# Kernel tuning notes

Measured on AMD Instinct MI355X. Metric: run time of the kernel, lower is better.

The kernel has to match this reference:

```python
import jax, jax.numpy as jnp
from jax import lax
import numpy as np

B, C, FH, FW, H, V, L = 256, 512, 8, 16, 512, 64, 24


def setup_inputs() -> dict:
    key = jax.random.key(0)
    ks = jax.random.split(key, 32)
    s = 0.05
    n = lambda k, shp: jax.random.normal(k, shp, dtype=jnp.float32) * s
    return {
        "encoder_ftrs": jax.random.normal(ks[0], (B, C, FH, FW), dtype=jnp.float32),
        "sequences": jax.random.randint(ks[1], (B, L), 0, V),
        "test": 0,
        "embed_w": n(ks[2], (V, H)),
        "init_state": n(ks[3], (2, 1, H)),
        "attn_W_w": n(ks[4], (H, C)), "attn_W_b": jnp.zeros((H,), jnp.float32),
        "attn_U_w": n(ks[5], (H, H)), "attn_U_b": jnp.zeros((H,), jnp.float32),
        "attn_v_w": n(ks[6], (1, H)), "attn_v_b": jnp.zeros((1,), jnp.float32),
        "fc_w": n(ks[7], (H, C + H)), "fc_b": jnp.zeros((H,), jnp.float32),
        "cls_w": n(ks[8], (V, H)), "cls_b": jnp.zeros((V,), jnp.float32),
        "gru0_wih": n(ks[9], (3 * H, 2 * H)), "gru0_whh": n(ks[10], (3 * H, H)),
        "gru0_bih": jnp.zeros((3 * H,), jnp.float32), "gru0_bhh": jnp.zeros((3 * H,), jnp.float32),
        "gru1_wih": n(ks[11], (3 * H, H)), "gru1_whh": n(ks[12], (3 * H, H)),
        "gru1_bih": jnp.zeros((3 * H,), jnp.float32), "gru1_bhh": jnp.zeros((3 * H,), jnp.float32),
    }


def _gru_cell(x, h, wih, whh, bih, bhh):
    # PyTorch GRUCell: r,z gates then candidate n with r applied on hidden path
    gi = x @ wih.T + bih
    gh = h @ whh.T + bhh
    i_r, i_z, i_n = jnp.split(gi, 3, axis=-1)
    h_r, h_z, h_n = jnp.split(gh, 3, axis=-1)
    r = jax.nn.sigmoid(i_r + h_r)
    z = jax.nn.sigmoid(i_z + h_z)
    nact = jnp.tanh(i_n + r * h_n)
    return (1.0 - z) * nact + z * h


def reference(encoder_ftrs, sequences, test, embed_w, init_state,
              attn_W_w, attn_W_b, attn_U_w, attn_U_b, attn_v_w, attn_v_b,
              fc_w, fc_b, cls_w, cls_b,
              gru0_wih, gru0_whh, gru0_bih, gru0_bhh,
              gru1_wih, gru1_whh, gru1_bih, gru1_bhh):
    bsz = encoder_ftrs.shape[0]
    # [B, L_sp, C] encoder states
    states = encoder_ftrs.reshape(bsz, C, -1).transpose(0, 2, 1)
    # attn_W(states) is timestep-independent: precompute once (same math)
    Ws = states @ attn_W_w.T + attn_W_b  # [B, L_sp, H]

    def apply_attn(h_top):
        e = jax.nn.relu(Ws + (h_top @ attn_U_w.T + attn_U_b)[:, None, :])
        scores = e @ attn_v_w[0] + attn_v_b[0]          # [B, L_sp]
        a = jax.nn.softmax(scores, axis=-1)
        ctx = jnp.einsum('bl,blc->bc', a, states)        # [B, C]
        return ctx

    def out_proj(ctx, h_top):
        return jax.nn.relu(jnp.concatenate([ctx, h_top], axis=-1) @ fc_w.T + fc_b)

    xs = embed_w[sequences[:, :-1]]                      # [B, T, H]
    h0 = jnp.broadcast_to(init_state, (2, bsz, H))       # repeat over batch
    y0 = out_proj(apply_attn(h0[1]), h0[1])              # time_step == -1 (output dropped)

    def step(carry, x_t):
        h, y = carry
        h_l0 = _gru_cell(jnp.concatenate([y, x_t], axis=-1), h[0],
                         gru0_wih, gru0_whh, gru0_bih, gru0_bhh)
        h_l1 = _gru_cell(h_l0, h[1], gru1_wih, gru1_whh, gru1_bih, gru1_bhh)
        hn = jnp.stack([h_l0, h_l1], axis=0)
        yn = out_proj(apply_attn(h_l1), h_l1)
        return (hn, yn), yn

    _, ys = lax.scan(step, (h0, y0), xs.transpose(1, 0, 2))   # [T, B, H]
    logits = ys.transpose(1, 0, 2) @ cls_w.T + cls_b          # [B, T, V]

    labels = sequences[:, 1:]
    mask = (labels > 0).astype(logits.dtype)
    logp = jax.nn.log_softmax(logits, axis=-1)
    nll = -jnp.take_along_axis(logp, labels[..., None], axis=-1)[..., 0]
    loss = jnp.sum(nll * mask) / jnp.sum(mask)
    return loss
```

## Files before the change

### kernel.cpp

```cpp
#include <hip/hip_runtime.h>
#include <hip/hip_bf16.h>
#include <cstddef>

#define BB 256
#define CC 512
#define SS 128
#define HH 512
#define VV 64
#define LL 24

typedef unsigned short ush;
typedef __attribute__((ext_vector_type(8))) short short8;
typedef __attribute__((ext_vector_type(4))) float f32x4;

__device__ __forceinline__ float wave_sum(float v) {
#pragma unroll
    for (int off = 32; off > 0; off >>= 1) v += __shfl_xor(v, off);
    return v;
}
__device__ __forceinline__ float wave_max(float v) {
#pragma unroll
    for (int off = 32; off > 0; off >>= 1) v = fmaxf(v, __shfl_xor(v, off));
    return v;
}
__device__ __forceinline__ float sigm(float x) { return 1.0f / (1.0f + expf(-x)); }
__device__ __forceinline__ ush f2bf(float f) {
    unsigned u = __float_as_uint(f);
    u += 0x7FFFu + ((u >> 16) & 1u);
    return (ush)(u >> 16);
}
__device__ __forceinline__ float bf2f(ush b) {
    return __uint_as_float(((unsigned)b) << 16);
}
__device__ __forceinline__ unsigned pack2(float a, float b) {
    return (unsigned)f2bf(a) | ((unsigned)f2bf(b) << 16);
}

__global__ __launch_bounds__(256) void init_kernel(const float* __restrict__ init_state,
                                                   float* __restrict__ h0,
                                                   float* __restrict__ h1,
                                                   ush* __restrict__ h0b,
                                                   ush* __restrict__ h1b,
                                                   float* __restrict__ acc) {
    int idx = blockIdx.x * 256 + threadIdx.x;
    if (idx < BB * HH) {
        float a = init_state[idx & (HH - 1)];
        float b = init_state[HH + (idx & (HH - 1))];
        h0[idx] = a; h1[idx] = b;
        h0b[idx] = f2bf(a); h1b[idx] = f2bf(b);
    }
    if (idx < 2) acc[idx] = 0.0f;
}

__global__ __launch_bounds__(256) void conv_kernel(const float* __restrict__ src,
                                                   ush* __restrict__ dst, int n4) {
    int i = blockIdx.x * 256 + threadIdx.x;
    if (i < n4) {
        float4 v = ((const float4*)src)[i];
        uint2 o;
        o.x = pack2(v.x, v.y);
        o.y = pack2(v.z, v.w);
        ((uint2*)dst)[i] = o;
    }
}

__global__ __launch_bounds__(128) void gather_kernel(const float* __restrict__ embed_w,
                                                     const int* __restrict__ seq,
                                                     ush* __restrict__ xall) {
    int item = blockIdx.x;
    int t = item >> 8, m = item & 255;
    int row = seq[m * LL + t];
    float4 v = ((const float4*)(embed_w + (size_t)row * HH))[threadIdx.x];
    uint2 o;
    o.x = pack2(v.x, v.y);
    o.y = pack2(v.z, v.w);
    ((uint2*)(xall + (size_t)item * HH))[threadIdx.x] = o;
}

__global__ __launch_bounds__(256) void enc_conv(const float* __restrict__ enc,
                                                ush* __restrict__ enc_t) {
    int b = blockIdx.x, cg = blockIdx.y;
    int c0 = cg * 128;
    __shared__ ush tile[128][130];
    const float* src = enc + ((size_t)b * 512 + c0) * 128;
#pragma unroll
    for (int i = 0; i < 16; i++) {
        int lin = i * 256 + threadIdx.x;
        int cl = lin >> 5, s4 = lin & 31;
        float4 v = ((const float4*)(src + (size_t)cl * 128))[s4];
        ush b0 = f2bf(v.x), b1 = f2bf(v.y), b2 = f2bf(v.z), b3 = f2bf(v.w);
        tile[s4 * 4 + 0][cl] = b0;
        tile[s4 * 4 + 1][cl] = b1;
        tile[s4 * 4 + 2][cl] = b2;
        tile[s4 * 4 + 3][cl] = b3;
    }
    __syncthreads();
#pragma unroll
    for (int i = 0; i < 16; i++) {
        int lin = i * 256 + threadIdx.x;
        int sl = lin >> 5, c4 = lin & 31;
        ush a0 = tile[sl][c4 * 4 + 0], a1 = tile[sl][c4 * 4 + 1];
        ush a2 = tile[sl][c4 * 4 + 2], a3 = tile[sl][c4 * 4 + 3];
        uint2 o;
        o.x = (unsigned)a0 | ((unsigned)a1 << 16);
        o.y = (unsigned)a2 | ((unsigned)a3 << 16);
        ((uint2*)(enc_t + ((size_t)b * 128 + sl) * 512 + c0))[c4] = o;
    }
}

__global__ __launch_bounds__(256) void ws_v2(const ush* __restrict__ enc_t,
                                             const ush* __restrict__ Wb,
                                             const float* __restrict__ bias,
                                             ush* __restrict__ Ws_bf) {
    int tid = threadIdx.x;
    int wave = tid >> 6, lane = tid & 63;
    int quad = lane >> 4, l16 = lane & 15;
    int m0 = blockIdx.x * 128 + wave * 32;
    int n0 = blockIdx.y * 128;
    const ush* ap = enc_t + (size_t)(m0 + l16) * 512 + quad * 8;
    const ush* bp = Wb + (size_t)(n0 + l16) * 512 + quad * 8;
    f32x4 acc[2][8];
#pragma unroll
    for (int f = 0; f < 2; f++)
#pragma unroll
        for (int s = 0; s < 8; s++) acc[f][s] = (f32x4){0.f, 0.f, 0.f, 0.f};
    short8 ac[2], bc[8], an[2], bn[8];
    ac[0] = *(const short8*)(ap);
    ac[1] = *(const short8*)(ap + (size_t)16 * 512);
#pragma unroll
    for (int s = 0; s < 8; s++) bc[s] = *(const short8*)(bp + (size_t)s * 16 * 512);
#pragma unroll
    for (int ks = 0; ks < 16; ks++) {
        if (ks < 15) {
            int k = (ks + 1) * 32;
            an[0] = *(const short8*)(ap + k);
            an[1] = *(const short8*)(ap + (size_t)16 * 512 + k);
#pragma unroll
            for (int s = 0; s < 8; s++)
                bn[s] = *(const short8*)(bp + (size_t)s * 16 * 512 + k);
        }
#pragma unroll
        for (int f = 0; f < 2; f++)
#pragma unroll
            for (int s = 0; s < 8; s++)
                acc[f][s] = __builtin_amdgcn_mfma_f32_16x16x32_bf16(ac[f], bc[s], acc[f][s], 0, 0, 0);
        if (ks < 15) {
            ac[0] = an[0]; ac[1] = an[1];
#pragma unroll
            for (int s = 0; s < 8; s++) bc[s] = bn[s];
        }
    }
#pragma unroll
    for (int s = 0; s < 8; s++) {
        int n = n0 + s * 16 + l16;
        float bs = bias[n];
#pragma unroll
        for (int f = 0; f < 2; f++)
#pragma unroll
            for (int r = 0; r < 4; r++) {
                int m = m0 + f * 16 + quad * 4 + r;
                Ws_bf[(size_t)m * HH + n] = f2bf(acc[f][s][r] + bs);
            }
    }
}

template <int NSTEP>
__device__ __forceinline__ void segk(const ush* __restrict__ ap,
                                     const ush* __restrict__ bp,
                                     size_t wofs, f32x4& a0, f32x4& a1) {
    short8 as[4], bs0[4], bs1[4];
    constexpr int PRE = NSTEP < 4 ? NSTEP : 4;
#pragma unroll
    for (int i = 0; i < PRE; i++) {
        as[i]  = *(const short8*)(ap + 32 * i);
        bs0[i] = *(const short8*)(bp + 32 * i);
        bs1[i] = *(const short8*)(bp + wofs + 32 * i);
    }
#pragma unroll
    for (int i = 0; i < NSTEP; i++) {
        const int sl = i & 3;
        a0 = __builtin_amdgcn_mfma_f32_16x16x32_bf16(as[sl], bs0[sl], a0, 0, 0, 0);
        a1 = __builtin_amdgcn_mfma_f32_16x16x32_bf16(as[sl], bs1[sl], a1, 0, 0, 0);
        if (i + 4 < NSTEP) {
            as[sl]  = *(const short8*)(ap + 32 * (i + 4));
            bs0[sl] = *(const short8*)(bp + 32 * (i + 4));
            bs1[sl] = *(const short8*)(bp + wofs + 32 * (i + 4));
        }
    }
}

struct GruArgs {
    const ush* xs[8][2];
    const ush* wb[8][2];
    int wst[8][2];
    int nks[8][2];
    int slot[8][2];
    int zmask;
};

__global__ __launch_bounds__(512) void gru_fused(GruArgs A,
                                                 const float* __restrict__ h_prev,
                                                 const float* __restrict__ bih,
                                                 const float* __restrict__ bhh,
                                                 float* __restrict__ h_out,
                                                 ush* __restrict__ h_out_bf) {
    int tid = threadIdx.x;
    int wave = __builtin_amdgcn_readfirstlane(tid >> 6);
    int lane = tid & 63, quad = lane >> 4, l16 = lane & 15;
    int m0 = blockIdx.x * 16, n0 = blockIdx.y * 32;
    __shared__ float gbuf[10][16][32];
    if (A.zmask) {
        int mi = tid >> 5, ni = tid & 31;
#pragma unroll
        for (int s = 0; s < 10; s++)
            if ((A.zmask >> s) & 1) gbuf[s][mi][ni] = 0.0f;
    }
    for (int e = 0; e < 2; e++) {
        int nks = A.nks[wave][e];
        if (nks == 0) continue;
        f32x4 a0 = (f32x4){0.f, 0.f, 0.f, 0.f};
        f32x4 a1 = (f32x4){0.f, 0.f, 0.f, 0.f};
        int wst = A.wst[wave][e];
        const ush* ap = A.xs[wave][e] + (size_t)(m0 + l16) * 512 + quad * 8;
        const ush* bp = A.wb[wave][e] + (size_t)(n0 + l16) * wst + quad * 8;
        size_t wofs = (size_t)16 * wst;
        if (nks == 16) segk<16>(ap, bp, wofs, a0, a1);
        else           segk<8>(ap, bp, wofs, a0, a1);
        int sl = A.slot[wave][e];
#pragma unroll
        for (int r = 0; r < 4; r++) {
            gbuf[sl][quad * 4 + r][l16]      = a0[r];
            gbuf[sl][quad * 4 + r][16 + l16] = a1[r];
        }
    }
    __syncthreads();
    {
        int mi = tid >> 5, ni = tid & 31;
        int n = n0 + ni;
        size_t off = (size_t)(m0 + mi) * HH + n;
        float r  = sigm(gbuf[0][mi][ni] + gbuf[1][mi][ni] + gbuf[2][mi][ni] +
                        bih[n] + bhh[n]);
        float zf = sigm(gbuf[3][mi][ni] + gbuf[4][mi][ni] + gbuf[5][mi][ni] +
                        bih[512 + n] + bhh[512 + n]);
        float na = tanhf(gbuf[6][mi][ni] + gbuf[7][mi][ni] + bih[1024 + n] +
                         r * (gbuf[8][mi][ni] + gbuf[9][mi][ni] + bhh[1024 + n]));
        float hp = h_prev[off];
        float ho = (1.0f - zf) * na + zf * hp;
        h_out[off] = ho;
        h_out_bf[off] = f2bf(ho);
    }
}

__global__ __launch_bounds__(512) void fc_fused(const ush* __restrict__ ctx,
                                                const ush* __restrict__ h,
                                                const ush* __restrict__ wFc,
                                                const float* __restrict__ bias,
                                                ush* __restrict__ y,
                                                ush* __restrict__ ys) {
    int tid = threadIdx.x;
    int wave = __builtin_amdgcn_readfirstlane(tid >> 6);
    int lane = tid & 63, quad = lane >> 4, l16 = lane & 15;
    int m0 = blockIdx.x * 16, n0 = blockIdx.y * 32;
    const ush* X = (wave < 4) ? ctx : h;
    int q = wave & 3;
    f32x4 a0 = (f32x4){0.f, 0.f, 0.f, 0.f};
    f32x4 a1 = (f32x4){0.f, 0.f, 0.f, 0.f};
    const ush* ap = X + (size_t)(m0 + l16) * 512 + q * 128 + quad * 8;
    const ush* bp = wFc + (size_t)(n0 + l16) * 1024 + (wave >= 4 ? 512 : 0) + q * 128 + quad * 8;
    segk<4>(ap, bp, (size_t)16 * 1024, a0, a1);
    __shared__ float gbuf[8][16][32];
#pragma unroll
    for (int r = 0; r < 4; r++) {
        gbuf[wave][quad * 4 + r][l16]      = a0[r];
        gbuf[wave][quad * 4 + r][16 + l16] = a1[r];
    }
    __syncthreads();
    {
        int mi = tid >> 5, ni = tid & 31;
        int n = n0 + ni;
        float v = bias[n];
#pragma unroll
        for (int w = 0; w < 8; w++) v += gbuf[w][mi][ni];
        v = fmaxf(v, 0.0f);
        ush bb = f2bf(v);
        size_t off = (size_t)(m0 + mi) * HH + n;
        y[off] = bb;
        if (ys) ys[off] = bb;
    }
}

__global__ __launch_bounds__(512) void u_fused(const ush* __restrict__ h,
                                               const ush* __restrict__ wU,
                                               const float* __restrict__ Ub,
                                               float* __restrict__ Uo) {
    int tid = threadIdx.x;
    int wave = __builtin_amdgcn_readfirstlane(tid >> 6);
    int lane = tid & 63, quad = lane >> 4, l16 = lane & 15;
    int m0 = blockIdx.x * 16, n0 = blockIdx.y * 32;
    f32x4 a0 = (f32x4){0.f, 0.f, 0.f, 0.f};
    f32x4 a1 = (f32x4){0.f, 0.f, 0.f, 0.f};
    const ush* ap = h + (size_t)(m0 + l16) * 512 + wave * 64 + quad * 8;
    const ush* bp = wU + (size_t)(n0 + l16) * 512 + wave * 64 + quad * 8;
    segk<2>(ap, bp, (size_t)16 * 512, a0, a1);
    __shared__ float gbuf[8][16][32];
#pragma unroll
    for (int r = 0; r < 4; r++) {
        gbuf[wave][quad * 4 + r][l16]      = a0[r];
        gbuf[wave][quad * 4 + r][16 + l16] = a1[r];
    }
    __syncthreads();
    {
        int mi = tid >> 5, ni = tid & 31;
        int n = n0 + ni;
        float v = Ub[n];
#pragma unroll
        for (int w = 0; w < 8; w++) v += gbuf[w][mi][ni];
        Uo[(size_t)(m0 + mi) * HH + n] = v;
    }
}

__global__ __launch_bounds__(512) void attn3(const float* __restrict__ u,
                                             const float* __restrict__ vw,
                                             const ush* __restrict__ Ws_bf,
                                             const ush* __restrict__ enc_t,
                                             ush* __restrict__ ctx_bf) {
    int b = blockIdx.x;
    int tid = threadIdx.x;
    int wave = tid >> 6, lane = tid & 63;
    int hi = lane >> 4, li = lane & 15;
    __shared__ float a[SS];
    __shared__ float part[8][512];

    float ur[4][8], vr[4][8];
#pragma unroll
    for (int p = 0; p < 4; p++) {
        const float* up = u + (size_t)b * HH + p * 128 + li * 8;
        const float* vp = vw + p * 128 + li * 8;
        float4 u0 = *(const float4*)(up);
        float4 u1 = *(const float4*)(up + 4);
        float4 v0 = *(const float4*)(vp);
        float4 v1 = *(const float4*)(vp + 4);
        ur[p][0] = u0.x; ur[p][1] = u0.y; ur[p][2] = u0.z; ur[p][3] = u0.w;
        ur[p][4] = u1.x; ur[p][5] = u1.y; ur[p][6] = u1.z; ur[p][7] = u1.w;
        vr[p][0] = v0.x; vr[p][1] = v0.y; vr[p][2] = v0.z; vr[p][3] = v0.w;
        vr[p][4] = v1.x; vr[p][5] = v1.y; vr[p][6] = v1.z; vr[p][7] = v1.w;
    }
    const ush* wsb = Ws_bf + (size_t)b * SS * HH;
#pragma unroll
    for (int pass = 0; pass < 4; pass++) {
        int s = pass * 32 + wave * 4 + hi;
        float acc = 0.0f;
#pragma unroll
        for (int p = 0; p < 4; p++) {
            short8 rv = *(const short8*)(wsb + (size_t)s * HH + p * 128 + li * 8);
#pragma unroll
            for (int j = 0; j < 8; j++) {
                float e = bf2f((ush)rv[j]) + ur[p][j];
                acc += fmaxf(e, 0.0f) * vr[p][j];
            }
        }
#pragma unroll
        for (int off = 1; off < 16; off <<= 1) acc += __shfl_xor(acc, off);
        if (li == 0) a[s] = acc;
    }
    __syncthreads();
    if (wave == 0) {
        float s0v = a[lane], s1v = a[lane + 64];
        float m = wave_max(fmaxf(s0v, s1v));
        float e0 = expf(s0v - m), e1 = expf(s1v - m);
        float ssum = wave_sum(e0 + e1);
        float inv = 1.0f / ssum;
        a[lane] = e0 * inv;
        a[lane + 64] = e1 * inv;
    }
    __syncthreads();
    float c8[8];
#pragma unroll
    for (int j = 0; j < 8; j++) c8[j] = 0.0f;
    const ush* ebt = enc_t + (size_t)b * SS * 512;
#pragma unroll
    for (int i = 0; i < 16; i++) {
        int s = wave * 16 + i;
        float as = a[s];
        short8 ev = *(const short8*)(ebt + (size_t)s * 512 + lane * 8);
#pragma unroll
        for (int j = 0; j < 8; j++) c8[j] += as * bf2f((ush)ev[j]);
    }
    *(float4*)(&part[wave][lane * 8])     = (float4){c8[0], c8[1], c8[2], c8[3]};
    *(float4*)(&part[wave][lane * 8 + 4]) = (float4){c8[4], c8[5], c8[6], c8[7]};
    __syncthreads();
    {
        float sum = 0.0f;
#pragma unroll
        for (int w = 0; w < 8; w++) sum += part[w][tid];
        ctx_bf[(size_t)b * CC + tid] = f2bf(sum);
    }
}

__global__ __launch_bounds__(256) void cls_fused(const ush* __restrict__ ys,
                                                 const ush* __restrict__ wCls,
                                                 const float* __restrict__ cls_b,
                                                 const int* __restrict__ seq,
                                                 float* __restrict__ acc) {
    int tid = threadIdx.x;
    int wave = tid >> 6, lane = tid & 63;
    int quad = lane >> 4, l16 = lane & 15;
    int m0 = blockIdx.x * 16;
    f32x4 a4[4];
#pragma unroll
    for (int s = 0; s < 4; s++) a4[s] = (f32x4){0.f, 0.f, 0.f, 0.f};
    const ush* ap = ys + (size_t)(m0 + l16) * 512 + wave * 128 + quad * 8;
    const ush* bp = wCls + (size_t)l16 * 512 + wave * 128 + quad * 8;
#pragma unroll
    for (int ks = 0; ks < 4; ks++) {
        short8 av = *(const short8*)(ap + ks * 32);
#pragma unroll
        for (int s = 0; s < 4; s++) {
            short8 bv = *(const short8*)(bp + (size_t)s * 16 * 512 + ks * 32);
            a4[s] = __builtin_amdgcn_mfma_f32_16x16x32_bf16(av, bv, a4[s], 0, 0, 0);
        }
    }
    __shared__ float gbuf[4][16][64];
    __shared__ float red[8];
#pragma unroll
    for (int s = 0; s < 4; s++)
#pragma unroll
        for (int r = 0; r < 4; r++)
            gbuf[wave][quad * 4 + r][s * 16 + l16] = a4[s][r];
    __syncthreads();
    float lsum = 0.0f, lcnt = 0.0f;
#pragma unroll
    for (int ii = 0; ii < 4; ii++) {
        int mi = wave * 4 + ii;
        int item = m0 + mi;
        int t = item >> 8, b = item & 255;
        float v = gbuf[0][mi][lane] + gbuf[1][mi][lane] + gbuf[2][mi][lane] +
                  gbuf[3][mi][lane] + cls_b[lane];
        float mx = wave_max(v);
        float e = expf(v - mx);
        float ssum = wave_sum(e);
        int label = seq[b * LL + t + 1];
        float vl = __shfl(v, label);
        if (label > 0) {
            lsum += -(vl - mx - logf(ssum));
            lcnt += 1.0f;
        }
    }
    if (lane == 0) { red[wave] = lsum; red[4 + wave] = lcnt; }
    __syncthreads();
    if (tid == 0) {
        atomicAdd(&acc[0], red[0] + red[1] + red[2] + red[3]);
        atomicAdd(&acc[1], red[4] + red[5] + red[6] + red[7]);
    }
}

__global__ void final_kernel(const float* __restrict__ acc, float* __restrict__ out) {
    if (threadIdx.x == 0) out[0] = acc[0] / acc[1];
}

extern "C" void kernel_launch(void* const* d_in, const int* in_sizes, int n_in,
                              void* d_out, int out_size, void* d_ws, size_t ws_size,
                              hipStream_t stream) {
    const float* enc        = (const float*)d_in[0];
    const int*   seq        = (const int*)d_in[1];
    const float* embed_w    = (const float*)d_in[3];
    const float* init_state = (const float*)d_in[4];
    const float* attn_W_w   = (const float*)d_in[5];
    const float* attn_W_b   = (const float*)d_in[6];
    const float* attn_U_w   = (const float*)d_in[7];
    const float* attn_U_b   = (const float*)d_in[8];
    const float* attn_v_w   = (const float*)d_in[9];
    const float* fc_w       = (const float*)d_in[11];
    const float* fc_b       = (const float*)d_in[12];
    const float* cls_w      = (const float*)d_in[13];
    const float* cls_b      = (const float*)d_in[14];
    const float* g0_wih     = (const float*)d_in[15];
    const float* g0_whh     = (const float*)d_in[16];
    const float* g0_bih     = (const float*)d_in[17];
    const float* g0_bhh     = (const float*)d_in[18];
    const float* g1_wih     = (const float*)d_in[19];
    const float* g1_whh     = (const float*)d_in[20];
    const float* g1_bih     = (const float*)d_in[21];
    const float* g1_bhh     = (const float*)d_in[22];
    float* out = (float*)d_out;

    float* ws = (float*)d_ws;
    size_t o = 0;
    ush* Ws_bf   = (ush*)(ws + o); o += (size_t)BB * SS * HH / 2;
    ush* enc_t   = (ush*)(ws + o); o += (size_t)BB * CC * SS / 2;
    ush* ys_bf   = (ush*)(ws + o); o += (size_t)(LL - 1) * BB * HH / 2;
    ush* xall_bf = (ush*)(ws + o); o += (size_t)(LL - 1) * BB * HH / 2;
    ush* wWb  = (ush*)(ws + o); o += 262144 / 2;
    ush* wU   = (ush*)(ws + o); o += 262144 / 2;
    ush* wFc  = (ush*)(ws + o); o += 524288 / 2;
    ush* wCls = (ush*)(ws + o); o += 32768 / 2;
    ush* wG0i = (ush*)(ws + o); o += 1572864 / 2;
    ush* wG0h = (ush*)(ws + o); o += 786432 / 2;
    ush* wG1i = (ush*)(ws + o); o += 786432 / 2;
    ush* wG1h = (ush*)(ws + o); o += 786432 / 2;
    float* Uo   = ws + o; o += (size_t)BB * HH;
    float* h0a  = ws + o; o += (size_t)BB * HH;
    float* h0b  = ws + o; o += (size_t)BB * HH;
    float* h1a  = ws + o; o += (size_t)BB * HH;
    float* h1b  = ws + o; o += (size_t)BB * HH;
    float* acc  = ws + o; o += 256;
    ush* h0a_bf = (ush*)(ws + o); o += (size_t)BB * HH / 2;
    ush* h0b_bf = (ush*)(ws + o); o += (size_t)BB * HH / 2;
    ush* h1a_bf = (ush*)(ws + o); o += (size_t)BB * HH / 2;
    ush* h1b_bf = (ush*)(ws + o); o += (size_t)BB * HH / 2;
    ush* y_bf   = (ush*)(ws + o); o += (size_t)BB * HH / 2;
    ush* ctx_bf = (ush*)(ws + o); o += (size_t)BB * CC / 2;

    init_kernel<<<512, 256, 0, stream>>>(init_state, h0a, h1a, h0a_bf, h1a_bf, acc);
    conv_kernel<<<256, 256, 0, stream>>>(attn_W_w, wWb, 65536);
    conv_kernel<<<256, 256, 0, stream>>>(attn_U_w, wU, 65536);
    conv_kernel<<<512, 256, 0, stream>>>(fc_w, wFc, 131072);
    conv_kernel<<<32, 256, 0, stream>>>(cls_w, wCls, 8192);
    conv_kernel<<<1536, 256, 0, stream>>>(g0_wih, wG0i, 393216);
    conv_kernel<<<768, 256, 0, stream>>>(g0_whh, wG0h, 196608);
    conv_kernel<<<768, 256, 0, stream>>>(g1_wih, wG1i, 196608);
    conv_kernel<<<768, 256, 0, stream>>>(g1_whh, wG1h, 196608);
    enc_conv<<<dim3(256, 4), 256, 0, stream>>>(enc, enc_t);
    gather_kernel<<<(LL - 1) * BB, 128, 0, stream>>>(embed_w, seq, xall_bf);
    ws_v2<<<dim3(256, 4), 256, 0, stream>>>(enc_t, wWb, attn_W_b, Ws_bf);

    auto setw = [](GruArgs& a, int w, int e, const ush* xs, const ush* wb,
                   int wst, int nks, int slot) {
        a.xs[w][e] = xs; a.wb[w][e] = wb; a.wst[w][e] = wst;
        a.nks[w][e] = nks; a.slot[w][e] = slot;
    };
    auto gru0_args = [&](const ush* y, const ush* x, const ush* h0) {
        GruArgs a{};
        setw(a, 0, 0, y,        wG0i,                             1024, 16, 0);
        setw(a, 1, 0, x,        wG0i + 512,                       1024, 16, 1);
        setw(a, 2, 0, h0,       wG0h,                              512, 16, 2);
        setw(a, 3, 0, y,        wG0i + (size_t)512 * 1024,        1024, 16, 3);
        setw(a, 4, 0, x,        wG0i + (size_t)512 * 1024 + 512,  1024, 16, 4);
        setw(a, 5, 0, h0,       wG0h + (size_t)512 * 512,          512, 16, 5);
        setw(a, 6, 0, y,        wG0i + (size_t)1024 * 1024,       1024, 16, 6);
        setw(a, 7, 0, x,        wG0i + (size_t)1024 * 1024 + 512, 1024, 16, 7);
        setw(a, 6, 1, h0,       wG0h + (size_t)1024 * 512,         512,  8, 8);
        setw(a, 7, 1, h0 + 256, wG0h + (size_t)1024 * 512 + 256,   512,  8, 9);
        a.zmask = 0;
        return a;
    };
    auto gru1_args = [&](const ush* hl0, const ush* h1) {
        GruArgs a{};
        setw(a, 0, 0, hl0,       wG1i,                             512, 16, 0);
        setw(a, 1, 0, h1,        wG1h,                             512, 16, 1);
        setw(a, 2, 0, hl0,       wG1i + (size_t)512 * 512,         512, 16, 3);
        setw(a, 3, 0, h1,        wG1h + (size_t)512 * 512,         512, 16, 4);
        setw(a, 4, 0, hl0,       wG1i + (size_t)1024 * 512,        512,  8, 6);
        setw(a, 5, 0, hl0 + 256, wG1i + (size_t)1024 * 512 + 256,  512,  8, 7);
        setw(a, 6, 0, h1,        wG1h + (size_t)1024 * 512,        512,  8, 8);
        setw(a, 7, 0, h1 + 256,  wG1h + (size_t)1024 * 512 + 256,  512,  8, 9);
        a.zmask = (1 << 2) | (1 << 5);
        return a;
    };

    u_fused<<<dim3(16, 16), 512, 0, stream>>>(h1a_bf, wU, attn_U_b, Uo);
    attn3<<<BB, 512, 0, stream>>>(Uo, attn_v_w, Ws_bf, enc_t, ctx_bf);
    fc_fused<<<dim3(16, 16), 512, 0, stream>>>(ctx_bf, h1a_bf, wFc, fc_b, y_bf, nullptr);

    float* h0_in = h0a; float* h0_out = h0b;
    float* h1_in = h1a; float* h1_out = h1b;
    ush* h0_in_bf = h0a_bf; ush* h0_out_bf = h0b_bf;
    ush* h1_in_bf = h1a_bf; ush* h1_out_bf = h1b_bf;
    for (int t = 0; t < LL - 1; t++) {
        gru_fused<<<dim3(16, 16), 512, 0, stream>>>(
            gru0_args(y_bf, xall_bf + (size_t)t * BB * HH, h0_in_bf),
            h0_in, g0_bih, g0_bhh, h0_out, h0_out_bf);
        gru_fused<<<dim3(16, 16), 512, 0, stream>>>(
            gru1_args(h0_out_bf, h1_in_bf),
            h1_in, g1_bih, g1_bhh, h1_out, h1_out_bf);
        u_fused<<<dim3(16, 16), 512, 0, stream>>>(h1_out_bf, wU, attn_U_b, Uo);
        attn3<<<BB, 512, 0, stream>>>(Uo, attn_v_w, Ws_bf, enc_t, ctx_bf);
        fc_fused<<<dim3(16, 16), 512, 0, stream>>>(ctx_bf, h1_out_bf, wFc, fc_b,
                                                   y_bf, ys_bf + (size_t)t * BB * HH);
        float* tmp;
        tmp = h0_in; h0_in = h0_out; h0_out = tmp;
        tmp = h1_in; h1_in = h1_out; h1_out = tmp;
        ush* tb;
        tb = h0_in_bf; h0_in_bf = h0_out_bf; h0_out_bf = tb;
        tb = h1_in_bf; h1_in_bf = h1_out_bf; h1_out_bf = tb;
    }

    cls_fused<<<368, 256, 0, stream>>>(ys_bf, wCls, cls_b, seq, acc);
    final_kernel<<<1, 1, 0, stream>>>(acc, out);
}
```

Baseline: 1.395 ms.

## Fuse attention U projection into attention kernel and batch weight conversions

Removes the separate u_fused MFMA kernel per timestep. The U projection is now computed inside the attention kernel, one block per batch row, as a scalar dot product over a transposed bf16 copy of attn_U_w read from global memory with fp32 h1 held in LDS. The seven per-weight conversion launches are merged into one multi-segment kernel, and the Ws GEMM now reads fp32 encoder features directly with strided loads. This cuts launches and the Uo round trip, but each of the 256 attention blocks rereads the whole U matrix without tensor cores, and the Ws A-operand loads are uncoalesced.

```diff
diff --git a/kernel.cpp b/kernel.cpp
--- a/kernel.cpp
+++ b/kernel.cpp
@@ -32,6 +32,8 @@
 __device__ __forceinline__ float bf2f(ush b) {
     return __uint_as_float(((unsigned)b) << 16);
 }
+__device__ __forceinline__ float bfl(unsigned u) { return __uint_as_float(u << 16); }
+__device__ __forceinline__ float bfh(unsigned u) { return __uint_as_float(u & 0xFFFF0000u); }
 __device__ __forceinline__ unsigned pack2(float a, float b) {
     return (unsigned)f2bf(a) | ((unsigned)f2bf(b) << 16);
 }
@@ -52,15 +54,50 @@
     if (idx < 2) acc[idx] = 0.0f;
 }
 
-__global__ __launch_bounds__(256) void conv_kernel(const float* __restrict__ src,
-                                                   ush* __restrict__ dst, int n4) {
-    int i = blockIdx.x * 256 + threadIdx.x;
-    if (i < n4) {
-        float4 v = ((const float4*)src)[i];
+struct CvArgs {
+    const float* src[7];
+    ush* dst[7];
+    int end[7];
+};
+__global__ __launch_bounds__(256) void conv_multi(CvArgs A) {
+    int blk = blockIdx.x;
+    int s = 0;
+    while (s < 6 && blk >= A.end[s]) s++;
+    int base = s ? A.end[s - 1] : 0;
+    int i = (blk - base) * 256 + threadIdx.x;
+    float4 v = ((const float4*)A.src[s])[i];
+    uint2 o;
+    o.x = pack2(v.x, v.y);
+    o.y = pack2(v.z, v.w);
+    ((uint2*)A.dst[s])[i] = o;
+}
+
+__global__ __launch_bounds__(256) void tp_conv(const float* __restrict__ src,
+                                               uint2* __restrict__ dst, int K) {
+    int n0 = blockIdx.x * 64, k0 = blockIdx.y * 64;
+    __shared__ ush til[64][68];
+    int tid = threadIdx.x;
+#pragma unroll
+    for (int i = 0; i < 4; i++) {
+        int idx = i * 256 + tid;
+        int r = idx >> 4, c4 = idx & 15;
+        float4 v = ((const float4*)(src + (size_t)(n0 + r) * K + k0))[c4];
+        til[r][c4 * 4 + 0] = f2bf(v.x);
+        til[r][c4 * 4 + 1] = f2bf(v.y);
+        til[r][c4 * 4 + 2] = f2bf(v.z);
+        til[r][c4 * 4 + 3] = f2bf(v.w);
+    }
+    __syncthreads();
+#pragma unroll
+    for (int i = 0; i < 4; i++) {
+        int idx = i * 256 + tid;
+        int k4l = idx >> 6, nl = idx & 63;
+        ush t0 = til[nl][k4l * 4 + 0], t1 = til[nl][k4l * 4 + 1];
+        ush t2 = til[nl][k4l * 4 + 2], t3 = til[nl][k4l * 4 + 3];
         uint2 o;
-        o.x = pack2(v.x, v.y);
-        o.y = pack2(v.z, v.w);
-        ((uint2*)dst)[i] = o;
+        o.x = (unsigned)t0 | ((unsigned)t1 << 16);
+        o.y = (unsigned)t2 | ((unsigned)t3 << 16);
+        dst[(size_t)(k0 / 4 + k4l) * 512 + n0 + nl] = o;
     }
 }
 
@@ -88,11 +125,10 @@
         int lin = i * 256 + threadIdx.x;
         int cl = lin >> 5, s4 = lin & 31;
         float4 v = ((const float4*)(src + (size_t)cl * 128))[s4];
-        ush b0 = f2bf(v.x), b1 = f2bf(v.y), b2 = f2bf(v.z), b3 = f2bf(v.w);
-        tile[s4 * 4 + 0][cl] = b0;
-        tile[s4 * 4 + 1][cl] = b1;
-        tile[s4 * 4 + 2][cl] = b2;
-        tile[s4 * 4 + 3][cl] = b3;
+        tile[s4 * 4 + 0][cl] = f2bf(v.x);
+        tile[s4 * 4 + 1][cl] = f2bf(v.y);
+        tile[s4 * 4 + 2][cl] = f2bf(v.z);
+        tile[s4 * 4 + 3][cl] = f2bf(v.w);
     }
     __syncthreads();
 #pragma unroll
@@ -108,60 +144,54 @@
     }
 }
 
-__global__ __launch_bounds__(256) void ws_v2(const ush* __restrict__ enc_t,
-                                             const ush* __restrict__ Wb,
-                                             const float* __restrict__ bias,
-                                             ush* __restrict__ Ws_bf) {
+__global__ __launch_bounds__(256) void ws_mfma(const float* __restrict__ enc,
+                                               const ush* __restrict__ Wb,
+                                               const float* __restrict__ bias,
+                                               ush* __restrict__ Ws_bf) {
     int tid = threadIdx.x;
     int wave = tid >> 6, lane = tid & 63;
     int quad = lane >> 4, l16 = lane & 15;
-    int m0 = blockIdx.x * 128 + wave * 32;
-    int n0 = blockIdx.y * 128;
-    const ush* ap = enc_t + (size_t)(m0 + l16) * 512 + quad * 8;
-    const ush* bp = Wb + (size_t)(n0 + l16) * 512 + quad * 8;
-    f32x4 acc[2][8];
-#pragma unroll
-    for (int f = 0; f < 2; f++)
-#pragma unroll
-        for (int s = 0; s < 8; s++) acc[f][s] = (f32x4){0.f, 0.f, 0.f, 0.f};
-    short8 ac[2], bc[8], an[2], bn[8];
-    ac[0] = *(const short8*)(ap);
-    ac[1] = *(const short8*)(ap + (size_t)16 * 512);
-#pragma unroll
-    for (int s = 0; s < 8; s++) bc[s] = *(const short8*)(bp + (size_t)s * 16 * 512);
-#pragma unroll
-    for (int ks = 0; ks < 16; ks++) {
-        if (ks < 15) {
-            int k = (ks + 1) * 32;
-            an[0] = *(const short8*)(ap + k);
-            an[1] = *(const short8*)(ap + (size_t)16 * 512 + k);
-#pragma unroll
-            for (int s = 0; s < 8; s++)
-                bn[s] = *(const short8*)(bp + (size_t)s * 16 * 512 + k);
-        }
-#pragma unroll
-        for (int f = 0; f < 2; f++)
-#pragma unroll
-            for (int s = 0; s < 8; s++)
-                acc[f][s] = __builtin_amdgcn_mfma_f32_16x16x32_bf16(ac[f], bc[s], acc[f][s], 0, 0, 0);
-        if (ks < 15) {
-            ac[0] = an[0]; ac[1] = an[1];
-#pragma unroll
-            for (int s = 0; s < 8; s++) bc[s] = bn[s];
-        }
-    }
-#pragma unroll
-    for (int s = 0; s < 8; s++) {
-        int n = n0 + s * 16 + l16;
-        float bs = bias[n];
-#pragma unroll
-        for (int f = 0; f < 2; f++)
+    int m0 = blockIdx.x * 256 + wave * 64;
+    int n0 = blockIdx.y * 64;
+    int b = m0 >> 7;
+    int s_base = m0 & 127;
+    const float* eb = enc + (size_t)b * CC * SS;
+    const ush* wp = Wb + (size_t)(n0 + l16) * 512 + quad * 8;
+    f32x4 acc[4][4];
+#pragma unroll
+    for (int f = 0; f < 4; f++)
+#pragma unroll
+        for (int s = 0; s < 4; s++) acc[f][s] = (f32x4){0.f, 0.f, 0.f, 0.f};
+    for (int k0 = 0; k0 < 512; k0 += 32) {
+        short8 af[4], bfr[4];
+#pragma unroll
+        for (int f = 0; f < 4; f++) {
+            int s = s_base + f * 16 + l16;
+#pragma unroll
+            for (int j = 0; j < 8; j++) {
+                float v = eb[(size_t)(k0 + quad * 8 + j) * SS + s];
+                af[f][j] = (short)f2bf(v);
+            }
+        }
+#pragma unroll
+        for (int s = 0; s < 4; s++)
+            bfr[s] = *(const short8*)(wp + (size_t)s * 16 * 512 + k0);
+#pragma unroll
+        for (int f = 0; f < 4; f++)
+#pragma unroll
+            for (int s = 0; s < 4; s++)
+                acc[f][s] = __builtin_amdgcn_mfma_f32_16x16x32_bf16(af[f], bfr[s], acc[f][s], 0, 0, 0);
+    }
+#pragma unroll
+    for (int f = 0; f < 4; f++)
+#pragma unroll
+        for (int s = 0; s < 4; s++)
 #pragma unroll
             for (int r = 0; r < 4; r++) {
                 int m = m0 + f * 16 + quad * 4 + r;
-                Ws_bf[(size_t)m * HH + n] = f2bf(acc[f][s][r] + bs);
+                int n = n0 + s * 16 + l16;
+                Ws_bf[(size_t)m * HH + n] = f2bf(acc[f][s][r] + bias[n]);
             }
-    }
 }
 
 template <int NSTEP>
@@ -213,7 +243,7 @@
         int mi = tid >> 5, ni = tid & 31;
 #pragma unroll
         for (int s = 0; s < 10; s++)
-            if ((A.zmask >> s) & 1) gbuf[s][mi][ni] = 0.0f;
+            if ((A.zmask >> s) & 1) gbuf[s][mi & 15][ni] = 0.0f;
     }
     for (int e = 0; e < 2; e++) {
         int nks = A.nks[wave][e];
@@ -235,7 +265,8 @@
     }
     __syncthreads();
     {
-        int mi = tid >> 5, ni = tid & 31;
+        int idx = tid;
+        int mi = idx >> 5, ni = idx & 31;
         int n = n0 + ni;
         size_t off = (size_t)(m0 + mi) * HH + n;
         float r  = sigm(gbuf[0][mi][ni] + gbuf[1][mi][ni] + gbuf[2][mi][ni] +
@@ -289,37 +320,9 @@
     }
 }
 
-__global__ __launch_bounds__(512) void u_fused(const ush* __restrict__ h,
-                                               const ush* __restrict__ wU,
-                                               const float* __restrict__ Ub,
-                                               float* __restrict__ Uo) {
-    int tid = threadIdx.x;
-    int wave = __builtin_amdgcn_readfirstlane(tid >> 6);
-    int lane = tid & 63, quad = lane >> 4, l16 = lane & 15;
-    int m0 = blockIdx.x * 16, n0 = blockIdx.y * 32;
-    f32x4 a0 = (f32x4){0.f, 0.f, 0.f, 0.f};
-    f32x4 a1 = (f32x4){0.f, 0.f, 0.f, 0.f};
-    const ush* ap = h + (size_t)(m0 + l16) * 512 + wave * 64 + quad * 8;
-    const ush* bp = wU + (size_t)(n0 + l16) * 512 + wave * 64 + quad * 8;
-    segk<2>(ap, bp, (size_t)16 * 512, a0, a1);
-    __shared__ float gbuf[8][16][32];
-#pragma unroll
-    for (int r = 0; r < 4; r++) {
-        gbuf[wave][quad * 4 + r][l16]      = a0[r];
-        gbuf[wave][quad * 4 + r][16 + l16] = a1[r];
-    }
-    __syncthreads();
-    {
-        int mi = tid >> 5, ni = tid & 31;
-        int n = n0 + ni;
-        float v = Ub[n];
-#pragma unroll
-        for (int w = 0; w < 8; w++) v += gbuf[w][mi][ni];
-        Uo[(size_t)(m0 + mi) * HH + n] = v;
-    }
-}
-
-__global__ __launch_bounds__(512) void attn3(const float* __restrict__ u,
+__global__ __launch_bounds__(512) void attn4(const float* __restrict__ h1f,
+                                             const uint2* __restrict__ wUt,
+                                             const float* __restrict__ Ub,
                                              const float* __restrict__ vw,
                                              const ush* __restrict__ Ws_bf,
                                              const ush* __restrict__ enc_t,
@@ -328,16 +331,34 @@
     int tid = threadIdx.x;
     int wave = tid >> 6, lane = tid & 63;
     int hi = lane >> 4, li = lane & 15;
+    __shared__ float h1s[512];
+    __shared__ float u_lds[512];
     __shared__ float a[SS];
     __shared__ float part[8][512];
 
+    h1s[tid] = h1f[(size_t)b * HH + tid];
+    __syncthreads();
+
+    {
+        float acc = Ub[tid];
+        const uint2* wp = wUt + tid;
+#pragma unroll 8
+        for (int kq = 0; kq < 128; kq++) {
+            uint2 pr = wp[(size_t)kq * 512];
+            float x0 = h1s[kq * 4 + 0], x1 = h1s[kq * 4 + 1];
+            float x2 = h1s[kq * 4 + 2], x3 = h1s[kq * 4 + 3];
+            acc += bfl(pr.x) * x0 + bfh(pr.x) * x1 + bfl(pr.y) * x2 + bfh(pr.y) * x3;
+        }
+        u_lds[tid] = acc;
+    }
+    __syncthreads();
+
     float ur[4][8], vr[4][8];
 #pragma unroll
     for (int p = 0; p < 4; p++) {
-        const float* up = u + (size_t)b * HH + p * 128 + li * 8;
+        float4 u0 = *(const float4*)(&u_lds[p * 128 + li * 8]);
+        float4 u1 = *(const float4*)(&u_lds[p * 128 + li * 8 + 4]);
         const float* vp = vw + p * 128 + li * 8;
-        float4 u0 = *(const float4*)(up);
-        float4 u1 = *(const float4*)(up + 4);
         float4 v0 = *(const float4*)(vp);
         float4 v1 = *(const float4*)(vp + 4);
         ur[p][0] = u0.x; ur[p][1] = u0.y; ur[p][2] = u0.z; ur[p][3] = u0.w;
@@ -364,6 +385,7 @@
         if (li == 0) a[s] = acc;
     }
     __syncthreads();
+
     if (wave == 0) {
         float s0v = a[lane], s1v = a[lane + 64];
         float m = wave_max(fmaxf(s0v, s1v));
@@ -374,20 +396,23 @@
         a[lane + 64] = e1 * inv;
     }
     __syncthreads();
-    float c8[8];
-#pragma unroll
-    for (int j = 0; j < 8; j++) c8[j] = 0.0f;
-    const ush* ebt = enc_t + (size_t)b * SS * 512;
-#pragma unroll
-    for (int i = 0; i < 16; i++) {
-        int s = wave * 16 + i;
-        float as = a[s];
-        short8 ev = *(const short8*)(ebt + (size_t)s * 512 + lane * 8);
-#pragma unroll
-        for (int j = 0; j < 8; j++) c8[j] += as * bf2f((ush)ev[j]);
-    }
-    *(float4*)(&part[wave][lane * 8])     = (float4){c8[0], c8[1], c8[2], c8[3]};
-    *(float4*)(&part[wave][lane * 8 + 4]) = (float4){c8[4], c8[5], c8[6], c8[7]};
+
+    {
+        float c8[8];
+#pragma unroll
+        for (int j = 0; j < 8; j++) c8[j] = 0.0f;
+        const ush* ebt = enc_t + (size_t)b * SS * 512;
+#pragma unroll
+        for (int i = 0; i < 16; i++) {
+            int s = wave * 16 + i;
+            float as = a[s];
+            short8 ev = *(const short8*)(ebt + (size_t)s * 512 + lane * 8);
+#pragma unroll
+            for (int j = 0; j < 8; j++) c8[j] += as * bf2f((ush)ev[j]);
+        }
+        *(float4*)(&part[wave][lane * 8])     = (float4){c8[0], c8[1], c8[2], c8[3]};
+        *(float4*)(&part[wave][lane * 8 + 4]) = (float4){c8[4], c8[5], c8[6], c8[7]};
+    }
     __syncthreads();
     {
         float sum = 0.0f;
@@ -491,14 +516,13 @@
     ush* ys_bf   = (ush*)(ws + o); o += (size_t)(LL - 1) * BB * HH / 2;
     ush* xall_bf = (ush*)(ws + o); o += (size_t)(LL - 1) * BB * HH / 2;
     ush* wWb  = (ush*)(ws + o); o += 262144 / 2;
-    ush* wU   = (ush*)(ws + o); o += 262144 / 2;
     ush* wFc  = (ush*)(ws + o); o += 524288 / 2;
     ush* wCls = (ush*)(ws + o); o += 32768 / 2;
     ush* wG0i = (ush*)(ws + o); o += 1572864 / 2;
     ush* wG0h = (ush*)(ws + o); o += 786432 / 2;
     ush* wG1i = (ush*)(ws + o); o += 786432 / 2;
     ush* wG1h = (ush*)(ws + o); o += 786432 / 2;
-    float* Uo   = ws + o; o += (size_t)BB * HH;
+    uint2* wUt = (uint2*)(ws + o); o += 131072;
     float* h0a  = ws + o; o += (size_t)BB * HH;
     float* h0b  = ws + o; o += (size_t)BB * HH;
     float* h1a  = ws + o; o += (size_t)BB * HH;
@@ -512,17 +536,23 @@
     ush* ctx_bf = (ush*)(ws + o); o += (size_t)BB * CC / 2;
 
     init_kernel<<<512, 256, 0, stream>>>(init_state, h0a, h1a, h0a_bf, h1a_bf, acc);
-    conv_kernel<<<256, 256, 0, stream>>>(attn_W_w, wWb, 65536);
-    conv_kernel<<<256, 256, 0, stream>>>(attn_U_w, wU, 65536);
-    conv_kernel<<<512, 256, 0, stream>>>(fc_w, wFc, 131072);
-    conv_kernel<<<32, 256, 0, stream>>>(cls_w, wCls, 8192);
-    conv_kernel<<<1536, 256, 0, stream>>>(g0_wih, wG0i, 393216);
-    conv_kernel<<<768, 256, 0, stream>>>(g0_whh, wG0h, 196608);
-    conv_kernel<<<768, 256, 0, stream>>>(g1_wih, wG1i, 196608);
-    conv_kernel<<<768, 256, 0, stream>>>(g1_whh, wG1h, 196608);
+    {
+        CvArgs cv{};
+        cv.src[0] = attn_W_w; cv.dst[0] = wWb;
+        cv.src[1] = fc_w;     cv.dst[1] = wFc;
+        cv.src[2] = cls_w;    cv.dst[2] = wCls;
+        cv.src[3] = g0_wih;   cv.dst[3] = wG0i;
+        cv.src[4] = g0_whh;   cv.dst[4] = wG0h;
+        cv.src[5] = g1_wih;   cv.dst[5] = wG1i;
+        cv.src[6] = g1_whh;   cv.dst[6] = wG1h;
+        cv.end[0] = 256;  cv.end[1] = 768;  cv.end[2] = 800;
+        cv.end[3] = 2336; cv.end[4] = 3104; cv.end[5] = 3872; cv.end[6] = 4640;
+        conv_multi<<<4640, 256, 0, stream>>>(cv);
+    }
+    tp_conv<<<dim3(8, 8), 256, 0, stream>>>(attn_U_w, wUt, 512);
     enc_conv<<<dim3(256, 4), 256, 0, stream>>>(enc, enc_t);
     gather_kernel<<<(LL - 1) * BB, 128, 0, stream>>>(embed_w, seq, xall_bf);
-    ws_v2<<<dim3(256, 4), 256, 0, stream>>>(enc_t, wWb, attn_W_b, Ws_bf);
+    ws_mfma<<<dim3(128, 8), 256, 0, stream>>>(enc, wWb, attn_W_b, Ws_bf);
 
     auto setw = [](GruArgs& a, int w, int e, const ush* xs, const ush* wb,
                    int wst, int nks, int slot) {
@@ -558,8 +588,7 @@
         return a;
     };
 
-    u_fused<<<dim3(16, 16), 512, 0, stream>>>(h1a_bf, wU, attn_U_b, Uo);
-    attn3<<<BB, 512, 0, stream>>>(Uo, attn_v_w, Ws_bf, enc_t, ctx_bf);
+    attn4<<<BB, 512, 0, stream>>>(h1a, wUt, attn_U_b, attn_v_w, Ws_bf, enc_t, ctx_bf);
     fc_fused<<<dim3(16, 16), 512, 0, stream>>>(ctx_bf, h1a_bf, wFc, fc_b, y_bf, nullptr);
 
     float* h0_in = h0a; float* h0_out = h0b;
@@ -573,8 +602,8 @@
         gru_fused<<<dim3(16, 16), 512, 0, stream>>>(
             gru1_args(h0_out_bf, h1_in_bf),
             h1_in, g1_bih, g1_bhh, h1_out, h1_out_bf);
-        u_fused<<<dim3(16, 16), 512, 0, stream>>>(h1_out_bf, wU, attn_U_b, Uo);
-        attn3<<<BB, 512, 0, stream>>>(Uo, attn_v_w, Ws_bf, enc_t, ctx_bf);
+        attn4<<<BB, 512, 0, stream>>>(h1_out, wUt, attn_U_b, attn_v_w, Ws_bf,
+                                      enc_t, ctx_bf);
         fc_fused<<<dim3(16, 16), 512, 0, stream>>>(ctx_bf, h1_out_bf, wFc, fc_b,
                                                    y_bf, ys_bf + (size_t)t * BB * HH);
         float* tmp;
```

New measurement: 1.485 ms. +6.4%, slower.
